# Kernel optimization log

Hardware: AMD Instinct MI355X
Metric: run time of the kernel (lower is better)

## Reference

```python
import jax, jax.numpy as jnp
import numpy as np

NB = 5  # frequency bands


def _ln(x, g, b, eps=1e-5):
    m = jnp.mean(x, axis=-1, keepdims=True)
    v = jnp.var(x, axis=-1, keepdims=True)
    return (x - m) / jnp.sqrt(v + eps) * g + b


def _graph_adj(x, adj_w, sw1, sb1, sw2, sb2, pos_factor, pos_enc):
    # x: [B, D, N] -> degree-normalized adjacency [B, N, N]
    d = x.shape[1]
    xt = jnp.swapaxes(x, 1, 2)  # [B, N, D]
    # concat-MLP first layer split: cat(xi, xj) @ W1 == xi @ W1[:d] + xj @ W1[d:]
    a = xt @ sw1[:d]
    bpart = xt @ sw1[d:]
    h = jax.nn.elu(a[:, :, None, :] + bpart[:, None, :, :] + sb1)  # [B, N, N, H]
    dyn = jax.nn.sigmoid(jnp.squeeze(h @ sw2, -1) + sb2)  # [B, N, N]
    static = jax.nn.softmax(adj_w, axis=-1)
    pos = jax.nn.softmax(pos_enc, axis=-1)
    comb = jax.nn.softmax(static + dyn + pos_factor * pos, axis=-1)
    deg = jnp.sum(comb, axis=-1)
    dis = (deg + 1e-8) ** -0.5
    return dis[:, :, None] * comb * dis[:, None, :]


def _gcn(x, adj, w, b):
    # x: [B, D, N], adj: [B, N, N] -> [B, D_out, N]
    xt = jnp.swapaxes(x, 1, 2)
    out = jnp.einsum('bij,bjd->bid', adj, xt) @ w + b
    return jnp.swapaxes(out, 1, 2)


def _mha(x, qkv_w, qkv_b, ow, ob, nh=4):
    B, S, D = x.shape
    dh = D // nh
    q, k, v = jnp.split(x @ qkv_w + qkv_b, 3, axis=-1)
    q = q.reshape(B, S, nh, dh)
    k = k.reshape(B, S, nh, dh)
    v = v.reshape(B, S, nh, dh)
    att = jax.nn.softmax(jnp.einsum('bihd,bjhd->bhij', q, k) / float(np.sqrt(dh)), axis=-1)
    o = jnp.einsum('bhij,bjhd->bihd', att, v).reshape(B, S, D)
    return o @ ow + ob


def setup_inputs():
    key = jax.random.key(0)
    B, D, N = 16, 256, 64
    ks = iter(jax.random.split(key, 40))

    def rn(shape, s=0.05):
        return jax.random.normal(next(ks), shape, dtype=jnp.float32) * s

    eyeN = jnp.eye(N, dtype=jnp.float32)
    return dict(
        feature=jax.random.normal(next(ks), (B, NB * D, 1, N), dtype=jnp.float32),
        l_adj_w=jnp.tile(eyeN[None], (NB, 1, 1)),
        l_sim_w1=rn((NB, 2 * D, D)), l_sim_b1=jnp.zeros((NB, D), jnp.float32),
        l_sim_w2=rn((NB, D, 1)), l_sim_b2=jnp.zeros((NB, 1), jnp.float32),
        l_pos_factor=jnp.full((NB,), 0.5, jnp.float32),
        l_pos_enc=jnp.tile(eyeN[None], (NB, 1, 1)),
        l_gcn_w=rn((NB, D, D)), l_gcn_b=jnp.zeros((NB, D), jnp.float32),
        g_adj_w=jnp.eye(NB, dtype=jnp.float32),
        g_sim_w1=rn((2 * D, D)), g_sim_b1=jnp.zeros((D,), jnp.float32),
        g_sim_w2=rn((D, 1)), g_sim_b2=jnp.zeros((1,), jnp.float32),
        g_pos_factor=jnp.float32(0.5),
        g_pos_enc=jnp.eye(NB, dtype=jnp.float32),
        g_gcn_w=rn((D, D)), g_gcn_b=jnp.zeros((D,), jnp.float32),
        qkv_w=rn((D, 3 * D)), qkv_b=jnp.zeros((3 * D,), jnp.float32),
        attn_ow=rn((D, D)), attn_ob=jnp.zeros((D,), jnp.float32),
        ln1_g=jnp.ones((D,), jnp.float32), ln1_b=jnp.zeros((D,), jnp.float32),
        ln2_g=jnp.ones((D,), jnp.float32), ln2_b=jnp.zeros((D,), jnp.float32),
        mlp_w1=rn((D, 4 * D)), mlp_b1=jnp.zeros((4 * D,), jnp.float32),
        mlp_w2=rn((4 * D, D)), mlp_b2=jnp.zeros((D,), jnp.float32),
        imp_w=rn((NB, N, 1)), imp_b=jnp.zeros((NB, 1), jnp.float32),
    )


def reference(feature, l_adj_w, l_sim_w1, l_sim_b1, l_sim_w2, l_sim_b2,
              l_pos_factor, l_pos_enc, l_gcn_w, l_gcn_b,
              g_adj_w, g_sim_w1, g_sim_b1, g_sim_w2, g_sim_b2,
              g_pos_factor, g_pos_enc, g_gcn_w, g_gcn_b,
              qkv_w, qkv_b, attn_ow, attn_ob,
              ln1_g, ln1_b, ln2_g, ln2_b,
              mlp_w1, mlp_b1, mlp_w2, mlp_b2,
              imp_w, imp_b):
    B = feature.shape[0]
    D = l_gcn_w.shape[-1]
    N = feature.shape[-1]
    # [B, 5*D, 1, N] -> [5, B, D, N] band-major
    x5 = jnp.moveaxis(feature.reshape(B, NB, D, N), 1, 0)
    # per-band local graphs + GCNs (vmapped over the 5 bands)
    local_adj = jax.vmap(_graph_adj)(x5, l_adj_w, l_sim_w1, l_sim_b1,
                                     l_sim_w2, l_sim_b2, l_pos_factor, l_pos_enc)
    local_out = jax.vmap(_gcn)(x5, local_adj, l_gcn_w, l_gcn_b)  # [5, B, D, N]
    scale_nodes = jnp.moveaxis(jnp.mean(local_out, axis=-1), 0, 1)  # [B, 5, D]
    # cross-band attention block (pre: MHA + residual + LN, then MLP + residual + LN)
    attn = _mha(scale_nodes, qkv_w, qkv_b, attn_ow, attn_ob)
    h1 = _ln(scale_nodes + attn, ln1_g, ln1_b)
    mlp = jax.nn.gelu(h1 @ mlp_w1 + mlp_b1, approximate=False) @ mlp_w2 + mlp_b2
    se = _ln(h1 + mlp, ln2_g, ln2_b)  # [B, 5, D]
    # global scale graph over the 5 band nodes
    xg = jnp.swapaxes(se, 1, 2)  # [B, D, 5]
    g_adj = _graph_adj(xg, g_adj_w, g_sim_w1, g_sim_b1, g_sim_w2, g_sim_b2,
                       g_pos_factor, g_pos_enc)
    g_out = jnp.swapaxes(_gcn(xg, g_adj, g_gcn_w, g_gcn_b), 1, 2)  # [B, 5, D]
    # modulate each local band feature by its global scale vector
    enh = local_out * jnp.moveaxis(g_out, 1, 0)[..., None]  # [5, B, D, N]
    # per-band importance projection over channels: [5, B, D, 1]
    out5 = jnp.einsum('kbdn,kno->kbdo', enh, imp_w) + imp_b[:, None, None, :]
    output = jnp.moveaxis(out5, 0, 1).reshape(B, NB * D, 1, 1)
    return output, g_adj, jnp.moveaxis(local_out, 0, 1)
```

## Files before the change

### kernel.cpp

```cpp
#include <hip/hip_runtime.h>
#include <hip/hip_bf16.h>

#define NBANDS 5
#define BATCH  16
#define DIM    256
#define NNODE  64
#define SEQ    5

typedef __hip_bfloat16 bf16;
typedef unsigned short ushort_t;
typedef __attribute__((ext_vector_type(8))) short short8;
typedef __attribute__((ext_vector_type(4))) float float4v;

#define MFMA __builtin_amdgcn_mfma_f32_16x16x32_bf16

__device__ __forceinline__ float bu2f(ushort_t u){
    bf16 h = *reinterpret_cast<bf16*>(&u);
    return __bfloat162float(h);
}
__device__ __forceinline__ ushort_t f2bu(float x){
    bf16 h = __float2bfloat16(x);
    return *reinterpret_cast<ushort_t*>(&h);
}
__device__ __forceinline__ float elu(float v){
    return (v > 0.f) ? v : (__expf(v) - 1.f);
}

__global__ void __launch_bounds__(256) k_head(
    const float* __restrict__ l_adj_w, const float* __restrict__ l_pos_enc,
    const float* __restrict__ l_pf,
    const float* __restrict__ g_adj_w, const float* __restrict__ g_pos_enc,
    const float* __restrict__ g_pf,
    float* __restrict__ sbase, float* __restrict__ gbase,
    const float* __restrict__ w1, const float* __restrict__ gw,
    ushort_t* __restrict__ w1bt, ushort_t* __restrict__ gwbt)
{
    int blk = blockIdx.x;
    int tid = threadIdx.x;
    __shared__ ushort_t tile[64][65];

    if (blk < 80) {
        int r = blk*4 + (tid>>6);
        int k = r >> 6, i = r & 63;
        int t = tid & 63;
        float aw = l_adj_w[(k*NNODE + i)*NNODE + t];
        float pe = l_pos_enc[(k*NNODE + i)*NNODE + t];
        float m1 = aw, m2 = pe;
        for (int o=32;o>0;o>>=1){ m1 = fmaxf(m1, __shfl_xor(m1,o,64)); m2 = fmaxf(m2, __shfl_xor(m2,o,64)); }
        float e1 = __expf(aw-m1), e2 = __expf(pe-m2);
        float s1=e1, s2=e2;
        for (int o=32;o>0;o>>=1){ s1 += __shfl_xor(s1,o,64); s2 += __shfl_xor(s2,o,64); }
        float pf = l_pf[k];
        sbase[(k*NNODE+i)*NNODE + t] = e1/s1 + pf*(e2/s2);
    } else if (blk == 80) {
        if (tid < NBANDS) {
            int i = tid;
            float r1[NBANDS], r2[NBANDS];
            float m1=-1e30f, m2=-1e30f;
            for (int j=0;j<NBANDS;j++){
                r1[j]=g_adj_w[i*NBANDS+j]; r2[j]=g_pos_enc[i*NBANDS+j];
                m1=fmaxf(m1,r1[j]); m2=fmaxf(m2,r2[j]);
            }
            float s1=0.f,s2=0.f;
            for (int j=0;j<NBANDS;j++){ r1[j]=__expf(r1[j]-m1); r2[j]=__expf(r2[j]-m2); s1+=r1[j]; s2+=r2[j]; }
            float pf = g_pf[0];
            for (int j=0;j<NBANDS;j++) gbase[i*NBANDS+j] = r1[j]/s1 + pf*(r2[j]/s2);
        }
    } else {
        int idx = blk - 81;
        int inst = idx >> 4;
        int t = idx & 15;
        int r0 = (t>>2)*64, c0 = (t&3)*64;
        const float* src; ushort_t* dst;
        if (inst < 10){
            int k = inst>>1, half = inst&1;
            src = w1  + ((size_t)k*512 + half*256)*256;
            dst = w1bt+ ((size_t)k*512 + half*256)*256;
        } else {
            int k = inst-10;
            src = gw  + (size_t)k*65536;
            dst = gwbt+ (size_t)k*65536;
        }
        int jj = tid & 63, i4 = tid >> 6;
        for (int p=0;p<16;p++){
            int i = p*4 + i4;
            tile[i][jj] = f2bu(src[(size_t)(r0+i)*256 + c0 + jj]);
        }
        __syncthreads();
        for (int p=0;p<16;p++){
            int i = p*4 + i4;
            dst[(size_t)(c0+i)*256 + r0 + jj] = tile[jj][i];
        }
    }
}

__global__ void __launch_bounds__(512) k_graph(
    const float* __restrict__ feat,
    const ushort_t* __restrict__ w1bt, const float* __restrict__ b1,
    const float* __restrict__ w2, const float* __restrict__ b2arr,
    const float* __restrict__ sbase,
    const ushort_t* __restrict__ gwbt, const float* __restrict__ gb,
    const float* __restrict__ imp_w,
    float* __restrict__ out_local,
    float* __restrict__ scalew4, float* __restrict__ impw4)
{
    int kb = blockIdx.x % 80;
    int iq = blockIdx.x / 80;
    int k  = kb >> 4;
    int b  = kb & 15;
    int i0 = iq << 4;
    int tid = threadIdx.x;
    int w = tid >> 6, lane = tid & 63, c16 = lane & 15, quad = lane >> 4;

    __shared__ ushort_t Ubuf[64*266 + 8];
    __shared__ ushort_t as[16][264];
    __shared__ ushort_t cs[16][72];
    __shared__ ushort_t ys[16][264];
    __shared__ float w2s[DIM];

    const float* src = feat + ((size_t)b*NBANDS + k)*DIM*NNODE;

    int il0 = w*2, il1 = w*2 + 1;
    float sb0 = sbase[(k*NNODE + i0 + il0)*NNODE + lane];
    float sb1 = sbase[(k*NNODE + i0 + il1)*NNODE + lane];
    float sbias2 = b2arr[k];

    if (tid < DIM) w2s[tid] = w2[k*DIM + tid];
    #pragma unroll
    for (int u = 0; u < 32; ++u){
        int idx = u*512 + tid;
        Ubuf[(idx & 63)*264 + (idx >> 6)] = f2bu(src[idx]);
    }
    __syncthreads();

    int col0 = w*32 + c16;
    int col1 = col0 + 16;

    const ushort_t* Ba = w1bt + (size_t)k*512*DIM;
    const ushort_t* Bb = Ba + 256*DIM;
    float4v z = {0.f,0.f,0.f,0.f};
    float4v aA0=z, aA1=z;
    float4v aB00=z,aB01=z,aB10=z,aB11=z,aB20=z,aB21=z,aB30=z,aB31=z;
    #pragma unroll
    for (int ks = 0; ks < 8; ++ks){
        int ko = ks*32 + quad*8;
        short8 fa = *reinterpret_cast<const short8*>(&Ubuf[(i0 + c16)*264 + ko]);
        short8 f0 = *reinterpret_cast<const short8*>(&Ubuf[( 0 + c16)*264 + ko]);
        short8 f1 = *reinterpret_cast<const short8*>(&Ubuf[(16 + c16)*264 + ko]);
        short8 f2 = *reinterpret_cast<const short8*>(&Ubuf[(32 + c16)*264 + ko]);
        short8 f3 = *reinterpret_cast<const short8*>(&Ubuf[(48 + c16)*264 + ko]);
        short8 wa0 = *reinterpret_cast<const short8*>(Ba + (size_t)col0*DIM + ko);
        short8 wa1 = *reinterpret_cast<const short8*>(Ba + (size_t)col1*DIM + ko);
        short8 wb0 = *reinterpret_cast<const short8*>(Bb + (size_t)col0*DIM + ko);
        short8 wb1 = *reinterpret_cast<const short8*>(Bb + (size_t)col1*DIM + ko);
        aA0  = MFMA(fa, wa0, aA0, 0,0,0);
        aA1  = MFMA(fa, wa1, aA1, 0,0,0);
        aB00 = MFMA(f0, wb0, aB00, 0,0,0);
        aB01 = MFMA(f0, wb1, aB01, 0,0,0);
        aB10 = MFMA(f1, wb0, aB10, 0,0,0);
        aB11 = MFMA(f1, wb1, aB11, 0,0,0);
        aB20 = MFMA(f2, wb0, aB20, 0,0,0);
        aB21 = MFMA(f2, wb1, aB21, 0,0,0);
        aB30 = MFMA(f3, wb0, aB30, 0,0,0);
        aB31 = MFMA(f3, wb1, aB31, 0,0,0);
    }
    __syncthreads();
    {
        float bias0 = b1[k*DIM + col0];
        float bias1 = b1[k*DIM + col1];
        int r0 = quad*4;
        #pragma unroll
        for (int r = 0; r < 4; ++r){
            as[r0 + r][col0] = f2bu(aA0[r] + bias0);
            as[r0 + r][col1] = f2bu(aA1[r] + bias1);
            Ubuf[( 0 + r0 + r)*266 + col0] = f2bu(aB00[r]);
            Ubuf[( 0 + r0 + r)*266 + col1] = f2bu(aB01[r]);
            Ubuf[(16 + r0 + r)*266 + col0] = f2bu(aB10[r]);
            Ubuf[(16 + r0 + r)*266 + col1] = f2bu(aB11[r]);
            Ubuf[(32 + r0 + r)*266 + col0] = f2bu(aB20[r]);
            Ubuf[(32 + r0 + r)*266 + col1] = f2bu(aB21[r]);
            Ubuf[(48 + r0 + r)*266 + col0] = f2bu(aB30[r]);
            Ubuf[(48 + r0 + r)*266 + col1] = f2bu(aB31[r]);
        }
    }
    __syncthreads();

    {
        const ushort_t* bd = Ubuf + 266*lane;
        const ushort_t* a0p = as[il0];
        const ushort_t* a1p = as[il1];
        float acc0 = 0.f, acc1 = 0.f;
        #pragma unroll 4
        for (int dd = 0; dd < 64; ++dd){
            unsigned int blo = *reinterpret_cast<const unsigned int*>(bd + dd*4);
            unsigned int bhi = *reinterpret_cast<const unsigned int*>(bd + dd*4 + 2);
            ushort4 a0 = *reinterpret_cast<const ushort4*>(a0p + dd*4);
            ushort4 a1 = *reinterpret_cast<const ushort4*>(a1p + dd*4);
            float4 wv  = *reinterpret_cast<const float4*>(&w2s[dd*4]);
            float bx = bu2f((ushort_t)(blo & 0xffffu));
            float by = bu2f((ushort_t)(blo >> 16));
            float bz = bu2f((ushort_t)(bhi & 0xffffu));
            float bq = bu2f((ushort_t)(bhi >> 16));
            acc0 += elu(bu2f(a0.x)+bx)*wv.x + elu(bu2f(a0.y)+by)*wv.y
                  + elu(bu2f(a0.z)+bz)*wv.z + elu(bu2f(a0.w)+bq)*wv.w;
            acc1 += elu(bu2f(a1.x)+bx)*wv.x + elu(bu2f(a1.y)+by)*wv.y
                  + elu(bu2f(a1.z)+bz)*wv.z + elu(bu2f(a1.w)+bq)*wv.w;
        }
        float sg0 = 1.f/(1.f + __expf(-(acc0 + sbias2)));
        float sg1 = 1.f/(1.f + __expf(-(acc1 + sbias2)));
        float val0 = sb0 + sg0;
        float val1 = sb1 + sg1;
        float m0 = val0, m1 = val1;
        for (int o=32;o>0;o>>=1){ m0 = fmaxf(m0, __shfl_xor(m0,o,64)); m1 = fmaxf(m1, __shfl_xor(m1,o,64)); }
        float e0 = __expf(val0 - m0), e1 = __expf(val1 - m1);
        float s0 = e0, s1 = e1;
        for (int o=32;o>0;o>>=1){ s0 += __shfl_xor(s0,o,64); s1 += __shfl_xor(s1,o,64); }
        cs[il0][lane] = f2bu(e0/s0);
        cs[il1][lane] = f2bu(e1/s1);
    }
    __syncthreads();

    float4v aY0 = z, aY1 = z;
    {
        #pragma unroll
        for (int ks = 0; ks < 2; ++ks){
            int ko = ks*32 + quad*8;
            short8 af = *reinterpret_cast<const short8*>(&cs[c16][ko]);
            const float* f0p = src + (size_t)col0*NNODE + ko;
            const float* f1p = src + (size_t)col1*NNODE + ko;
            float4 x0 = *reinterpret_cast<const float4*>(f0p);
            float4 x1 = *reinterpret_cast<const float4*>(f0p+4);
            float4 y0 = *reinterpret_cast<const float4*>(f1p);
            float4 y1 = *reinterpret_cast<const float4*>(f1p+4);
            short8 bf0, bf1;
            bf0[0]=(short)f2bu(x0.x); bf0[1]=(short)f2bu(x0.y); bf0[2]=(short)f2bu(x0.z); bf0[3]=(short)f2bu(x0.w);
            bf0[4]=(short)f2bu(x1.x); bf0[5]=(short)f2bu(x1.y); bf0[6]=(short)f2bu(x1.z); bf0[7]=(short)f2bu(x1.w);
            bf1[0]=(short)f2bu(y0.x); bf1[1]=(short)f2bu(y0.y); bf1[2]=(short)f2bu(y0.z); bf1[3]=(short)f2bu(y0.w);
            bf1[4]=(short)f2bu(y1.x); bf1[5]=(short)f2bu(y1.y); bf1[6]=(short)f2bu(y1.z); bf1[7]=(short)f2bu(y1.w);
            aY0 = MFMA(af, bf0, aY0, 0,0,0);
            aY1 = MFMA(af, bf1, aY1, 0,0,0);
        }
        #pragma unroll
        for (int r=0;r<4;++r){
            ys[quad*4 + r][col0] = f2bu(aY0[r]);
            ys[quad*4 + r][col1] = f2bu(aY1[r]);
        }
    }
    __syncthreads();

    {
        float4v aG0 = z, aG1 = z;
        const ushort_t* Bg = gwbt + (size_t)k*DIM*DIM;
        #pragma unroll
        for (int ks = 0; ks < 8; ++ks){
            int ko = ks*32 + quad*8;
            short8 af = *reinterpret_cast<const short8*>(&ys[c16][ko]);
            short8 g0 = *reinterpret_cast<const short8*>(Bg + (size_t)col0*DIM + ko);
            short8 g1 = *reinterpret_cast<const short8*>(Bg + (size_t)col1*DIM + ko);
            aG0 = MFMA(af, g0, aG0, 0,0,0);
            aG1 = MFMA(af, g1, aG1, 0,0,0);
        }
        int nb = i0 + quad*4;
        float iw0 = imp_w[k*NNODE + nb + 0];
        float iw1 = imp_w[k*NNODE + nb + 1];
        float iw2 = imp_w[k*NNODE + nb + 2];
        float iw3 = imp_w[k*NNODE + nb + 3];
        size_t obase = ((size_t)b*NBANDS + k)*DIM;

        float bias0 = gb[k*DIM + col0];
        float v0 = aG0[0]+bias0, v1 = aG0[1]+bias0, v2 = aG0[2]+bias0, v3 = aG0[3]+bias0;
        float4 vv = make_float4(v0,v1,v2,v3);
        *reinterpret_cast<float4*>(&out_local[(obase + col0)*NNODE + nb]) = vv;
        float s  = v0+v1+v2+v3;
        float di = v0*iw0 + v1*iw1 + v2*iw2 + v3*iw3;
        s  += __shfl_xor(s,16,64);  s  += __shfl_xor(s,32,64);
        di += __shfl_xor(di,16,64); di += __shfl_xor(di,32,64);
        if (quad == 0){
            size_t o = ((size_t)iq*80 + b*SEQ + k)*DIM + col0;
            scalew4[o] = s;
            impw4[o]   = di;
        }

        float bias1 = gb[k*DIM + col1];
        v0 = aG1[0]+bias1; v1 = aG1[1]+bias1; v2 = aG1[2]+bias1; v3 = aG1[3]+bias1;
        vv = make_float4(v0,v1,v2,v3);
        *reinterpret_cast<float4*>(&out_local[(obase + col1)*NNODE + nb]) = vv;
        s  = v0+v1+v2+v3;
        di = v0*iw0 + v1*iw1 + v2*iw2 + v3*iw3;
        s  += __shfl_xor(s,16,64);  s  += __shfl_xor(s,32,64);
        di += __shfl_xor(di,16,64); di += __shfl_xor(di,32,64);
        if (quad == 0){
            size_t o = ((size_t)iq*80 + b*SEQ + k)*DIM + col1;
            scalew4[o] = s;
            impw4[o]   = di;
        }
    }
}

__global__ void __launch_bounds__(256) k_qkv_gemv(const float* __restrict__ scalew4,
                        const float* __restrict__ w, const float* __restrict__ bias,
                        float* __restrict__ out)
{
    int row = blockIdx.x / 12;
    int n0 = (blockIdx.x % 12) * 64;
    int tid = threadIdx.x;
    int c = tid & 63, s = tid >> 6;
    __shared__ float xs[DIM];
    __shared__ float part[4][64];
    {
        size_t basei = (size_t)row*DIM + tid;
        xs[tid] = (scalew4[basei] + scalew4[20480 + basei]
                 + scalew4[40960 + basei] + scalew4[61440 + basei]) * (1.f/64.f);
    }
    __syncthreads();
    const float* wp = w + (size_t)(s*64)*768 + n0 + c;
    const float* xp = xs + s*64;
    float acc = 0.f;
    #pragma unroll 8
    for (int i = 0; i < 64; ++i) acc += xp[i] * wp[(size_t)i*768];
    part[s][c] = acc;
    __syncthreads();
    if (s == 0){
        out[(size_t)row*768 + n0 + c] = bias[n0+c] + part[0][c]+part[1][c]+part[2][c]+part[3][c];
    }
}

template<int COLS, int SLICES>
__global__ void __launch_bounds__(256) k_gemv(const float* __restrict__ x, const float* __restrict__ w,
                       const float* __restrict__ bias, float* __restrict__ out,
                       int K, int N, int act)
{
    int chunks = N / COLS;
    int row = blockIdx.x / chunks;
    int n0 = (blockIdx.x % chunks) * COLS;
    int c = threadIdx.x % COLS, s = threadIdx.x / COLS;
    __shared__ float xs[1024];
    __shared__ float part[SLICES][COLS];
    for (int i = threadIdx.x; i < K; i += 256) xs[i] = x[(size_t)row*K + i];
    __syncthreads();
    int klen = K / SLICES;
    const float* wp = w + (size_t)(s*klen)*N + n0 + c;
    const float* xp = xs + s*klen;
    float acc = 0.f;
    #pragma unroll 8
    for (int i = 0; i < klen; ++i) acc += xp[i] * wp[(size_t)i*N];
    part[s][c] = acc;
    __syncthreads();
    if (s == 0){
        float v = bias[n0+c];
        #pragma unroll
        for (int q=0;q<SLICES;q++) v += part[q][c];
        if (act) v = 0.5f*v*(1.f + erff(v*0.70710678118654752f));
        out[(size_t)row*N + n0 + c] = v;
    }
}

__global__ void __launch_bounds__(256) k_projattn(const float* __restrict__ qkvw,
                        const float* __restrict__ ow, const float* __restrict__ ob,
                        float* __restrict__ projw)
{
    int row = blockIdx.x / 4;
    int n0 = (blockIdx.x % 4) * 64;
    int b = row / SEQ, i = row % SEQ;
    int tid = threadIdx.x;
    int h = tid >> 6, l = tid & 63;
    __shared__ float xs[DIM];
    __shared__ float part[4][64];
    const float* base = qkvw + (size_t)b*SEQ*3*DIM;
    float qv = base[(size_t)i*3*DIM + h*64 + l];
    float pj[SEQ];
    #pragma unroll
    for (int j=0;j<SEQ;j++){
        float p = qv * base[(size_t)j*3*DIM + DIM + h*64 + l];
        for (int o=32;o>0;o>>=1) p += __shfl_xor(p,o,64);
        pj[j] = p * 0.125f;
    }
    float m = pj[0];
    #pragma unroll
    for (int j=1;j<SEQ;j++) m = fmaxf(m, pj[j]);
    float ssum = 0.f;
    #pragma unroll
    for (int j=0;j<SEQ;j++){ pj[j] = __expf(pj[j]-m); ssum += pj[j]; }
    float inv = 1.f/ssum;
    float o = 0.f;
    #pragma unroll
    for (int j=0;j<SEQ;j++) o += pj[j]*inv * base[(size_t)j*3*DIM + 2*DIM + h*64 + l];
    xs[tid] = o;
    __syncthreads();
    int c = tid & 63, s = tid >> 6;
    const float* wp = ow + (size_t)(s*64)*DIM + n0 + c;
    const float* xp = xs + s*64;
    float acc = 0.f;
    #pragma unroll 8
    for (int k=0;k<64;++k) acc += xp[k] * wp[(size_t)k*DIM];
    part[s][c] = acc;
    __syncthreads();
    if (s == 0){
        projw[(size_t)row*DIM + n0 + c] = ob[n0+c] + part[0][c]+part[1][c]+part[2][c]+part[3][c];
    }
}

__device__ __forceinline__ float block_ln(float v, int tid, float* red, float g, float bln)
{
    float s = v;
    for (int o=32;o>0;o>>=1) s += __shfl_xor(s,o,64);
    int wave = tid>>6, lane = tid&63;
    if (lane==0) red[wave] = s;
    __syncthreads();
    float mean = (red[0]+red[1]+red[2]+red[3]) * (1.f/DIM);
    float c = v - mean;
    float q = c*c;
    for (int o=32;o>0;o>>=1) q += __shfl_xor(q,o,64);
    __syncthreads();
    if (lane==0) red[wave] = q;
    __syncthreads();
    float var = (red[0]+red[1]+red[2]+red[3]) * (1.f/DIM);
    return c * rsqrtf(var + 1e-5f) * g + bln;
}

__global__ void __launch_bounds__(256) k_mlp1_ln(const float* __restrict__ projw,
                         const float* __restrict__ scalew4,
                         const float* __restrict__ ln1_g, const float* __restrict__ ln1_b,
                         const float* __restrict__ w1, const float* __restrict__ b1,
                         float* __restrict__ h1w, float* __restrict__ mhw)
{
    int row = blockIdx.x / 16;
    int n0 = (blockIdx.x % 16) * 64;
    int tid = threadIdx.x;
    __shared__ float xs[DIM];
    __shared__ float red[4];
    __shared__ float part[4][64];
    size_t basei = (size_t)row*DIM + tid;
    float sc = (scalew4[basei] + scalew4[20480 + basei]
              + scalew4[40960 + basei] + scalew4[61440 + basei]) * (1.f/64.f);
    float v = projw[basei] + sc;
    float h = block_ln(v, tid, red, ln1_g[tid], ln1_b[tid]);
    xs[tid] = h;
    if ((blockIdx.x % 16) == 0) h1w[basei] = h;
    __syncthreads();
    int c = tid & 63, s = tid >> 6;
    const float* wp = w1 + (size_t)(s*64)*1024 + n0 + c;
    const float* xp = xs + s*64;
    float acc = 0.f;
    #pragma unroll 8
    for (int i=0;i<64;++i) acc += xp[i] * wp[(size_t)i*1024];
    part[s][c] = acc;
    __syncthreads();
    if (s == 0){
        float o = b1[n0+c] + part[0][c] + part[1][c] + part[2][c] + part[3][c];
        o = 0.5f*o*(1.f + erff(o*0.70710678118654752f));
        mhw[(size_t)row*1024 + n0 + c] = o;
    }
}

__global__ void __launch_bounds__(256) k_gab_ln(const float* __restrict__ m2w,
                        const float* __restrict__ h1w,
                        const float* __restrict__ ln2_g, const float* __restrict__ ln2_b,
                        const float* __restrict__ gw1, const float* __restrict__ gb1,
                        float* __restrict__ sew, float* __restrict__ gaw, float* __restrict__ gbw)
{
    int row = blockIdx.x / 4;
    int n0 = (blockIdx.x % 4) * 64;
    int tid = threadIdx.x;
    __shared__ float xs[DIM];
    __shared__ float red[4];
    __shared__ float partA[4][64];
    __shared__ float partB[4][64];
    float v = m2w[(size_t)row*DIM + tid] + h1w[(size_t)row*DIM + tid];
    float h = block_ln(v, tid, red, ln2_g[tid], ln2_b[tid]);
    xs[tid] = h;
    if ((blockIdx.x % 4) == 0) sew[(size_t)row*DIM + tid] = h;
    __syncthreads();
    int c = tid & 63, s = tid >> 6;
    const float* wpA = gw1 + (size_t)(s*64)*DIM + n0 + c;
    const float* wpB = wpA + (size_t)DIM*DIM;
    const float* xp = xs + s*64;
    float aA = 0.f, aB = 0.f;
    #pragma unroll 8
    for (int i=0;i<64;++i){
        float xv = xp[i];
        aA += xv * wpA[(size_t)i*DIM];
        aB += xv * wpB[(size_t)i*DIM];
    }
    partA[s][c] = aA;
    partB[s][c] = aB;
    __syncthreads();
    if (s == 0){
        gaw[(size_t)row*DIM + n0 + c] = gb1[n0+c] + partA[0][c]+partA[1][c]+partA[2][c]+partA[3][c];
        gbw[(size_t)row*DIM + n0 + c] = partB[0][c]+partB[1][c]+partB[2][c]+partB[3][c];
    }
}

__global__ void __launch_bounds__(256) k_goutfin(const float* __restrict__ gaw,
                        const float* __restrict__ gbw,
                        const float* __restrict__ gw2, const float* __restrict__ gb2,
                        const float* __restrict__ gbase,
                        const float* __restrict__ sew,
                        const float* __restrict__ ggw, const float* __restrict__ ggb,
                        const float* __restrict__ impw4, const float* __restrict__ imp_b,
                        float* __restrict__ out0, float* __restrict__ out_gadj)
{
    int row = blockIdx.x / 4;
    int n0 = (blockIdx.x % 4) * 64;
    int b = row / SEQ, i = row % SEQ;
    int tid = threadIdx.x;
    int wave = tid >> 6, lane = tid & 63;
    __shared__ float dyn_s[SEQ];
    __shared__ float xs[DIM];
    __shared__ float part[4][64];
    for (int j = wave; j < SEQ; j += 4){
        const float* gar = gaw + (size_t)row*DIM;
        const float* gbr = gbw + ((size_t)b*SEQ + j)*DIM;
        float acc = 0.f;
        #pragma unroll
        for (int m=0;m<4;m++){
            int dd = lane + m*64;
            float v = gar[dd] + gbr[dd];
            acc += elu(v) * gw2[dd];
        }
        for (int o=32;o>0;o>>=1) acc += __shfl_xor(acc,o,64);
        if (lane==0) dyn_s[j] = acc;
    }
    __syncthreads();
    float gc[SEQ];
    {
        float sb2 = gb2[0];
        float m = -1e30f;
        #pragma unroll
        for (int j=0;j<SEQ;j++){
            float sg = 1.f/(1.f+__expf(-(dyn_s[j]+sb2)));
            gc[j] = gbase[i*SEQ+j] + sg;
            m = fmaxf(m, gc[j]);
        }
        float ssum=0.f;
        #pragma unroll
        for (int j=0;j<SEQ;j++){ gc[j]=__expf(gc[j]-m); ssum+=gc[j]; }
        float inv = 1.f/ssum;
        #pragma unroll
        for (int j=0;j<SEQ;j++) gc[j] *= inv;
    }
    if (n0 == 0 && tid < SEQ) out_gadj[((size_t)b*SEQ+i)*SEQ + tid] = gc[tid];
    float t = 0.f;
    #pragma unroll
    for (int j=0;j<SEQ;j++) t += gc[j]*sew[((size_t)b*SEQ + j)*DIM + tid];
    xs[tid] = t;
    __syncthreads();
    int c = tid & 63, s = tid >> 6;
    const float* wp = ggw + (size_t)(s*64)*DIM + n0 + c;
    const float* xp = xs + s*64;
    float acc = 0.f;
    #pragma unroll 8
    for (int k=0;k<64;++k) acc += xp[k] * wp[(size_t)k*DIM];
    part[s][c] = acc;
    __syncthreads();
    if (s == 0){
        float g = ggb[n0+c] + part[0][c]+part[1][c]+part[2][c]+part[3][c];
        size_t o = (size_t)row*DIM + n0 + c;
        float imps = impw4[o] + impw4[20480 + o] + impw4[40960 + o] + impw4[61440 + o];
        out0[o] = g * imps + imp_b[i];
    }
}

extern "C" void kernel_launch(void* const* d_in, const int* in_sizes, int n_in,
                              void* d_out, int out_size, void* d_ws, size_t ws_size,
                              hipStream_t stream)
{
    const float* feature      = (const float*)d_in[0];
    const float* l_adj_w      = (const float*)d_in[1];
    const float* l_sim_w1     = (const float*)d_in[2];
    const float* l_sim_b1     = (const float*)d_in[3];
    const float* l_sim_w2     = (const float*)d_in[4];
    const float* l_sim_b2     = (const float*)d_in[5];
    const float* l_pos_factor = (const float*)d_in[6];
    const float* l_pos_enc    = (const float*)d_in[7];
    const float* l_gcn_w      = (const float*)d_in[8];
    const float* l_gcn_b      = (const float*)d_in[9];
    const float* g_adj_w      = (const float*)d_in[10];
    const float* g_sim_w1     = (const float*)d_in[11];
    const float* g_sim_b1     = (const float*)d_in[12];
    const float* g_sim_w2     = (const float*)d_in[13];
    const float* g_sim_b2     = (const float*)d_in[14];
    const float* g_pos_factor = (const float*)d_in[15];
    const float* g_pos_enc    = (const float*)d_in[16];
    const float* g_gcn_w      = (const float*)d_in[17];
    const float* g_gcn_b      = (const float*)d_in[18];
    const float* qkv_w        = (const float*)d_in[19];
    const float* qkv_b        = (const float*)d_in[20];
    const float* attn_ow      = (const float*)d_in[21];
    const float* attn_ob      = (const float*)d_in[22];
    const float* ln1_g        = (const float*)d_in[23];
    const float* ln1_b        = (const float*)d_in[24];
    const float* ln2_g        = (const float*)d_in[25];
    const float* ln2_b        = (const float*)d_in[26];
    const float* mlp_w1       = (const float*)d_in[27];
    const float* mlp_b1       = (const float*)d_in[28];
    const float* mlp_w2       = (const float*)d_in[29];
    const float* mlp_b2       = (const float*)d_in[30];
    const float* imp_w        = (const float*)d_in[31];
    const float* imp_b        = (const float*)d_in[32];

    float* out0      = (float*)d_out;
    float* out_gadj  = out0 + (size_t)BATCH*NBANDS*DIM;
    float* out_local = out_gadj + (size_t)BATCH*NBANDS*NBANDS;

    ushort_t* w1bt = (ushort_t*)d_ws;
    ushort_t* gwbt = w1bt + (size_t)NBANDS*512*DIM;
    float* fp = (float*)(gwbt + (size_t)NBANDS*DIM*DIM);
    float* sbase   = fp; fp += NBANDS*NNODE*NNODE;
    float* gbase   = fp; fp += 32;
    float* scalew4 = fp; fp += 4*BATCH*SEQ*DIM;
    float* impw4   = fp; fp += 4*BATCH*SEQ*DIM;
    float* qkvw    = fp; fp += BATCH*SEQ*3*DIM;
    float* projw   = fp; fp += BATCH*SEQ*DIM;
    float* h1w     = fp; fp += BATCH*SEQ*DIM;
    float* mhw     = fp; fp += BATCH*SEQ*4*DIM;
    float* m2w     = fp; fp += BATCH*SEQ*DIM;
    float* sew     = fp; fp += BATCH*SEQ*DIM;
    float* gaw     = fp; fp += BATCH*SEQ*DIM;
    float* gbw     = fp; fp += BATCH*SEQ*DIM;

    const int ROWS = BATCH*SEQ;

    k_head<<<321, 256, 0, stream>>>(l_adj_w, l_pos_enc, l_pos_factor,
                                    g_adj_w, g_pos_enc, g_pos_factor,
                                    sbase, gbase,
                                    l_sim_w1, l_gcn_w, w1bt, gwbt);
    k_graph<<<NBANDS*BATCH*4, 512, 0, stream>>>(feature, w1bt, l_sim_b1,
                                    l_sim_w2, l_sim_b2, sbase,
                                    gwbt, l_gcn_b, imp_w,
                                    out_local, scalew4, impw4);
    k_qkv_gemv<<<ROWS*12, 256, 0, stream>>>(scalew4, qkv_w, qkv_b, qkvw);
    k_projattn<<<ROWS*4, 256, 0, stream>>>(qkvw, attn_ow, attn_ob, projw);
    k_mlp1_ln<<<ROWS*16, 256, 0, stream>>>(projw, scalew4, ln1_g, ln1_b, mlp_w1, mlp_b1, h1w, mhw);
    k_gemv<32,8><<<ROWS*8, 256, 0, stream>>>(mhw, mlp_w2, mlp_b2, m2w, 1024, 256, 0);
    k_gab_ln<<<ROWS*4, 256, 0, stream>>>(m2w, h1w, ln2_g, ln2_b, g_sim_w1, g_sim_b1, sew, gaw, gbw);
    k_goutfin<<<ROWS*4, 256, 0, stream>>>(gaw, gbw, g_sim_w2, g_sim_b2, gbase,
                                          sew, g_gcn_w, g_gcn_b, impw4, imp_b,
                                          out0, out_gadj);
}
```

Measured before the change: 215.8 us.

## Pretranspose features to bf16 in head kernel and split graph rows into eighths

Adds a k_head stage that transposes and converts each band's feature slab to bf16 [N,D] in workspace. k_graph then reads MFMA operands directly from global memory instead of staging them through shared memory. k_graph now handles 8 query rows per block instead of 16, which doubles the grid to 640 blocks, and the partial sums grow from 4 to 8 slices that downstream kernels reduce. The intent is more parallelism and less per-block staging, at the cost of redundant B-part MFMA work per block, half-wasted MFMA tiles, and extra global traffic.

```diff
diff --git a/kernel.cpp b/kernel.cpp
--- a/kernel.cpp
+++ b/kernel.cpp
@@ -24,6 +24,12 @@
 }
 __device__ __forceinline__ float elu(float v){
     return (v > 0.f) ? v : (__expf(v) - 1.f);
+}
+__device__ __forceinline__ float sum8(const float* __restrict__ p, size_t i){
+    float v = 0.f;
+    #pragma unroll
+    for (int q = 0; q < 8; ++q) v += p[(size_t)q*20480 + i];
+    return v;
 }
 
 __global__ void __launch_bounds__(256) k_head(
@@ -33,7 +39,8 @@
     const float* __restrict__ g_pf,
     float* __restrict__ sbase, float* __restrict__ gbase,
     const float* __restrict__ w1, const float* __restrict__ gw,
-    ushort_t* __restrict__ w1bt, ushort_t* __restrict__ gwbt)
+    ushort_t* __restrict__ w1bt, ushort_t* __restrict__ gwbt,
+    const float* __restrict__ feat, ushort_t* __restrict__ xtb)
 {
     int blk = blockIdx.x;
     int tid = threadIdx.x;
@@ -66,7 +73,7 @@
             float pf = g_pf[0];
             for (int j=0;j<NBANDS;j++) gbase[i*NBANDS+j] = r1[j]/s1 + pf*(r2[j]/s2);
         }
-    } else {
+    } else if (blk < 321) {
         int idx = blk - 81;
         int inst = idx >> 4;
         int t = idx & 15;
@@ -91,51 +98,64 @@
             int i = p*4 + i4;
             dst[(size_t)(c0+i)*256 + r0 + jj] = tile[jj][i];
         }
+    } else {
+        int idx = blk - 321;
+        int k = idx >> 6;
+        int b = (idx >> 2) & 15;
+        int dt = idx & 3;
+        const float* src = feat + ((size_t)b*NBANDS*DIM + (size_t)k*DIM)*NNODE;
+        ushort_t* dst = xtb + (size_t)(k*BATCH+b)*NNODE*DIM;
+        for (int r=0;r<16;r++){
+            int dp = r*4 + (tid>>6);
+            int n  = tid & 63;
+            tile[dp][n] = f2bu(src[(size_t)(dt*64+dp)*NNODE + n]);
+        }
+        __syncthreads();
+        for (int r=0;r<16;r++){
+            int n  = r*4 + (tid>>6);
+            int dp = tid & 63;
+            dst[(size_t)n*DIM + dt*64 + dp] = tile[dp][n];
+        }
     }
 }
 
 __global__ void __launch_bounds__(512) k_graph(
-    const float* __restrict__ feat,
+    const float* __restrict__ feat, const ushort_t* __restrict__ xtb,
     const ushort_t* __restrict__ w1bt, const float* __restrict__ b1,
     const float* __restrict__ w2, const float* __restrict__ b2arr,
     const float* __restrict__ sbase,
     const ushort_t* __restrict__ gwbt, const float* __restrict__ gb,
     const float* __restrict__ imp_w,
     float* __restrict__ out_local,
-    float* __restrict__ scalew4, float* __restrict__ impw4)
+    float* __restrict__ scalew8, float* __restrict__ impw8)
 {
     int kb = blockIdx.x % 80;
     int iq = blockIdx.x / 80;
     int k  = kb >> 4;
     int b  = kb & 15;
-    int i0 = iq << 4;
+    int i0 = iq << 3;
     int tid = threadIdx.x;
     int w = tid >> 6, lane = tid & 63, c16 = lane & 15, quad = lane >> 4;
 
-    __shared__ ushort_t Ubuf[64*266 + 8];
-    __shared__ ushort_t as[16][264];
+    __shared__ ushort_t as[8][266];
+    __shared__ ushort_t bs[64][266];
     __shared__ ushort_t cs[16][72];
     __shared__ ushort_t ys[16][264];
-    __shared__ float w2s[DIM];
+
+    if (tid < 288) reinterpret_cast<unsigned int*>(&cs[8][0])[tid] = 0u;
+    for (int t = tid; t < 1056; t += 512) reinterpret_cast<unsigned int*>(&ys[8][0])[t] = 0u;
+
+    float sb = sbase[(k*NNODE + i0 + w)*NNODE + lane];
+    float sbias2 = b2arr[k];
 
     const float* src = feat + ((size_t)b*NBANDS + k)*DIM*NNODE;
-
-    int il0 = w*2, il1 = w*2 + 1;
-    float sb0 = sbase[(k*NNODE + i0 + il0)*NNODE + lane];
-    float sb1 = sbase[(k*NNODE + i0 + il1)*NNODE + lane];
-    float sbias2 = b2arr[k];
-
-    if (tid < DIM) w2s[tid] = w2[k*DIM + tid];
-    #pragma unroll
-    for (int u = 0; u < 32; ++u){
-        int idx = u*512 + tid;
-        Ubuf[(idx & 63)*264 + (idx >> 6)] = f2bu(src[idx]);
-    }
-    __syncthreads();
+    const ushort_t* X = xtb + (size_t)(k*BATCH + b)*NNODE*DIM;
 
     int col0 = w*32 + c16;
     int col1 = col0 + 16;
 
+    int arow = i0 + c16; if (arow > 63) arow = 63;
+    const ushort_t* Xa = X + (size_t)arow*DIM;
     const ushort_t* Ba = w1bt + (size_t)k*512*DIM;
     const ushort_t* Bb = Ba + 256*DIM;
     float4v z = {0.f,0.f,0.f,0.f};
@@ -144,11 +164,11 @@
     #pragma unroll
     for (int ks = 0; ks < 8; ++ks){
         int ko = ks*32 + quad*8;
-        short8 fa = *reinterpret_cast<const short8*>(&Ubuf[(i0 + c16)*264 + ko]);
-        short8 f0 = *reinterpret_cast<const short8*>(&Ubuf[( 0 + c16)*264 + ko]);
-        short8 f1 = *reinterpret_cast<const short8*>(&Ubuf[(16 + c16)*264 + ko]);
-        short8 f2 = *reinterpret_cast<const short8*>(&Ubuf[(32 + c16)*264 + ko]);
-        short8 f3 = *reinterpret_cast<const short8*>(&Ubuf[(48 + c16)*264 + ko]);
+        short8 fa = *reinterpret_cast<const short8*>(Xa + ko);
+        short8 f0 = *reinterpret_cast<const short8*>(X + (size_t)( 0 + c16)*DIM + ko);
+        short8 f1 = *reinterpret_cast<const short8*>(X + (size_t)(16 + c16)*DIM + ko);
+        short8 f2 = *reinterpret_cast<const short8*>(X + (size_t)(32 + c16)*DIM + ko);
+        short8 f3 = *reinterpret_cast<const short8*>(X + (size_t)(48 + c16)*DIM + ko);
         short8 wa0 = *reinterpret_cast<const short8*>(Ba + (size_t)col0*DIM + ko);
         short8 wa1 = *reinterpret_cast<const short8*>(Ba + (size_t)col1*DIM + ko);
         short8 wb0 = *reinterpret_cast<const short8*>(Bb + (size_t)col0*DIM + ko);
@@ -164,64 +184,62 @@
         aB30 = MFMA(f3, wb0, aB30, 0,0,0);
         aB31 = MFMA(f3, wb1, aB31, 0,0,0);
     }
-    __syncthreads();
     {
         float bias0 = b1[k*DIM + col0];
         float bias1 = b1[k*DIM + col1];
         int r0 = quad*4;
+        if (quad < 2){
+            #pragma unroll
+            for (int r = 0; r < 4; ++r){
+                as[r0 + r][col0] = f2bu(aA0[r] + bias0);
+                as[r0 + r][col1] = f2bu(aA1[r] + bias1);
+            }
+        }
         #pragma unroll
         for (int r = 0; r < 4; ++r){
-            as[r0 + r][col0] = f2bu(aA0[r] + bias0);
-            as[r0 + r][col1] = f2bu(aA1[r] + bias1);
-            Ubuf[( 0 + r0 + r)*266 + col0] = f2bu(aB00[r]);
-            Ubuf[( 0 + r0 + r)*266 + col1] = f2bu(aB01[r]);
-            Ubuf[(16 + r0 + r)*266 + col0] = f2bu(aB10[r]);
-            Ubuf[(16 + r0 + r)*266 + col1] = f2bu(aB11[r]);
-            Ubuf[(32 + r0 + r)*266 + col0] = f2bu(aB20[r]);
-            Ubuf[(32 + r0 + r)*266 + col1] = f2bu(aB21[r]);
-            Ubuf[(48 + r0 + r)*266 + col0] = f2bu(aB30[r]);
-            Ubuf[(48 + r0 + r)*266 + col1] = f2bu(aB31[r]);
+            bs[ 0 + r0 + r][col0] = f2bu(aB00[r]);
+            bs[ 0 + r0 + r][col1] = f2bu(aB01[r]);
+            bs[16 + r0 + r][col0] = f2bu(aB10[r]);
+            bs[16 + r0 + r][col1] = f2bu(aB11[r]);
+            bs[32 + r0 + r][col0] = f2bu(aB20[r]);
+            bs[32 + r0 + r][col1] = f2bu(aB21[r]);
+            bs[48 + r0 + r][col0] = f2bu(aB30[r]);
+            bs[48 + r0 + r][col1] = f2bu(aB31[r]);
         }
     }
     __syncthreads();
 
     {
-        const ushort_t* bd = Ubuf + 266*lane;
-        const ushort_t* a0p = as[il0];
-        const ushort_t* a1p = as[il1];
-        float acc0 = 0.f, acc1 = 0.f;
+        const ushort_t* bd = bs[lane];
+        const ushort_t* ap = as[w];
+        const float* w2p = w2 + k*DIM;
+        float acc = 0.f;
         #pragma unroll 4
         for (int dd = 0; dd < 64; ++dd){
             unsigned int blo = *reinterpret_cast<const unsigned int*>(bd + dd*4);
             unsigned int bhi = *reinterpret_cast<const unsigned int*>(bd + dd*4 + 2);
-            ushort4 a0 = *reinterpret_cast<const ushort4*>(a0p + dd*4);
-            ushort4 a1 = *reinterpret_cast<const ushort4*>(a1p + dd*4);
-            float4 wv  = *reinterpret_cast<const float4*>(&w2s[dd*4]);
+            ushort4 a0 = *reinterpret_cast<const ushort4*>(ap + dd*4);
+            float4 wv  = *reinterpret_cast<const float4*>(w2p + dd*4);
             float bx = bu2f((ushort_t)(blo & 0xffffu));
             float by = bu2f((ushort_t)(blo >> 16));
             float bz = bu2f((ushort_t)(bhi & 0xffffu));
             float bq = bu2f((ushort_t)(bhi >> 16));
-            acc0 += elu(bu2f(a0.x)+bx)*wv.x + elu(bu2f(a0.y)+by)*wv.y
-                  + elu(bu2f(a0.z)+bz)*wv.z + elu(bu2f(a0.w)+bq)*wv.w;
-            acc1 += elu(bu2f(a1.x)+bx)*wv.x + elu(bu2f(a1.y)+by)*wv.y
-                  + elu(bu2f(a1.z)+bz)*wv.z + elu(bu2f(a1.w)+bq)*wv.w;
-        }
-        float sg0 = 1.f/(1.f + __expf(-(acc0 + sbias2)));
-        float sg1 = 1.f/(1.f + __expf(-(acc1 + sbias2)));
-        float val0 = sb0 + sg0;
-        float val1 = sb1 + sg1;
-        float m0 = val0, m1 = val1;
-        for (int o=32;o>0;o>>=1){ m0 = fmaxf(m0, __shfl_xor(m0,o,64)); m1 = fmaxf(m1, __shfl_xor(m1,o,64)); }
-        float e0 = __expf(val0 - m0), e1 = __expf(val1 - m1);
-        float s0 = e0, s1 = e1;
-        for (int o=32;o>0;o>>=1){ s0 += __shfl_xor(s0,o,64); s1 += __shfl_xor(s1,o,64); }
-        cs[il0][lane] = f2bu(e0/s0);
-        cs[il1][lane] = f2bu(e1/s1);
-    }
-    __syncthreads();
-
-    float4v aY0 = z, aY1 = z;
+            acc += elu(bu2f(a0.x)+bx)*wv.x + elu(bu2f(a0.y)+by)*wv.y
+                 + elu(bu2f(a0.z)+bz)*wv.z + elu(bu2f(a0.w)+bq)*wv.w;
+        }
+        float sg = 1.f/(1.f + __expf(-(acc + sbias2)));
+        float val = sb + sg;
+        float m = val;
+        for (int o=32;o>0;o>>=1) m = fmaxf(m, __shfl_xor(m,o,64));
+        float e = __expf(val - m);
+        float s = e;
+        for (int o=32;o>0;o>>=1) s += __shfl_xor(s,o,64);
+        cs[w][lane] = f2bu(e/s);
+    }
+    __syncthreads();
+
     {
+        float4v aY0 = z, aY1 = z;
         #pragma unroll
         for (int ks = 0; ks < 2; ++ks){
             int ko = ks*32 + quad*8;
@@ -240,10 +258,12 @@
             aY0 = MFMA(af, bf0, aY0, 0,0,0);
             aY1 = MFMA(af, bf1, aY1, 0,0,0);
         }
-        #pragma unroll
-        for (int r=0;r<4;++r){
-            ys[quad*4 + r][col0] = f2bu(aY0[r]);
-            ys[quad*4 + r][col1] = f2bu(aY1[r]);
+        if (quad < 2){
+            #pragma unroll
+            for (int r=0;r<4;++r){
+                ys[quad*4 + r][col0] = f2bu(aY0[r]);
+                ys[quad*4 + r][col1] = f2bu(aY1[r]);
+            }
         }
     }
     __syncthreads();
@@ -261,43 +281,48 @@
             aG1 = MFMA(af, g1, aG1, 0,0,0);
         }
         int nb = i0 + quad*4;
-        float iw0 = imp_w[k*NNODE + nb + 0];
-        float iw1 = imp_w[k*NNODE + nb + 1];
-        float iw2 = imp_w[k*NNODE + nb + 2];
-        float iw3 = imp_w[k*NNODE + nb + 3];
+        int nbc = (quad < 2) ? nb : i0;
+        float iw0 = imp_w[k*NNODE + nbc + 0];
+        float iw1 = imp_w[k*NNODE + nbc + 1];
+        float iw2 = imp_w[k*NNODE + nbc + 2];
+        float iw3 = imp_w[k*NNODE + nbc + 3];
         size_t obase = ((size_t)b*NBANDS + k)*DIM;
 
         float bias0 = gb[k*DIM + col0];
         float v0 = aG0[0]+bias0, v1 = aG0[1]+bias0, v2 = aG0[2]+bias0, v3 = aG0[3]+bias0;
-        float4 vv = make_float4(v0,v1,v2,v3);
-        *reinterpret_cast<float4*>(&out_local[(obase + col0)*NNODE + nb]) = vv;
-        float s  = v0+v1+v2+v3;
-        float di = v0*iw0 + v1*iw1 + v2*iw2 + v3*iw3;
+        if (quad < 2){
+            *reinterpret_cast<float4*>(&out_local[(obase + col0)*NNODE + nb]) =
+                make_float4(v0,v1,v2,v3);
+        }
+        float s  = (quad < 2) ? (v0+v1+v2+v3) : 0.f;
+        float di = (quad < 2) ? (v0*iw0 + v1*iw1 + v2*iw2 + v3*iw3) : 0.f;
         s  += __shfl_xor(s,16,64);  s  += __shfl_xor(s,32,64);
         di += __shfl_xor(di,16,64); di += __shfl_xor(di,32,64);
         if (quad == 0){
-            size_t o = ((size_t)iq*80 + b*SEQ + k)*DIM + col0;
-            scalew4[o] = s;
-            impw4[o]   = di;
+            size_t o = (size_t)iq*20480 + ((size_t)b*SEQ + k)*DIM + col0;
+            scalew8[o] = s;
+            impw8[o]   = di;
         }
 
         float bias1 = gb[k*DIM + col1];
         v0 = aG1[0]+bias1; v1 = aG1[1]+bias1; v2 = aG1[2]+bias1; v3 = aG1[3]+bias1;
-        vv = make_float4(v0,v1,v2,v3);
-        *reinterpret_cast<float4*>(&out_local[(obase + col1)*NNODE + nb]) = vv;
-        s  = v0+v1+v2+v3;
-        di = v0*iw0 + v1*iw1 + v2*iw2 + v3*iw3;
+        if (quad < 2){
+            *reinterpret_cast<float4*>(&out_local[(obase + col1)*NNODE + nb]) =
+                make_float4(v0,v1,v2,v3);
+        }
+        s  = (quad < 2) ? (v0+v1+v2+v3) : 0.f;
+        di = (quad < 2) ? (v0*iw0 + v1*iw1 + v2*iw2 + v3*iw3) : 0.f;
         s  += __shfl_xor(s,16,64);  s  += __shfl_xor(s,32,64);
         di += __shfl_xor(di,16,64); di += __shfl_xor(di,32,64);
         if (quad == 0){
-            size_t o = ((size_t)iq*80 + b*SEQ + k)*DIM + col1;
-            scalew4[o] = s;
-            impw4[o]   = di;
-        }
-    }
-}
-
-__global__ void __launch_bounds__(256) k_qkv_gemv(const float* __restrict__ scalew4,
+            size_t o = (size_t)iq*20480 + ((size_t)b*SEQ + k)*DIM + col1;
+            scalew8[o] = s;
+            impw8[o]   = di;
+        }
+    }
+}
+
+__global__ void __launch_bounds__(256) k_qkv_gemv(const float* __restrict__ scalew8,
                         const float* __restrict__ w, const float* __restrict__ bias,
                         float* __restrict__ out)
 {
@@ -307,11 +332,7 @@
     int c = tid & 63, s = tid >> 6;
     __shared__ float xs[DIM];
     __shared__ float part[4][64];
-    {
-        size_t basei = (size_t)row*DIM + tid;
-        xs[tid] = (scalew4[basei] + scalew4[20480 + basei]
-                 + scalew4[40960 + basei] + scalew4[61440 + basei]) * (1.f/64.f);
-    }
+    xs[tid] = sum8(scalew8, (size_t)row*DIM + tid) * (1.f/64.f);
     __syncthreads();
     const float* wp = w + (size_t)(s*64)*768 + n0 + c;
     const float* xp = xs + s*64;
@@ -419,7 +440,7 @@
 }
 
 __global__ void __launch_bounds__(256) k_mlp1_ln(const float* __restrict__ projw,
-                         const float* __restrict__ scalew4,
+                         const float* __restrict__ scalew8,
                          const float* __restrict__ ln1_g, const float* __restrict__ ln1_b,
                          const float* __restrict__ w1, const float* __restrict__ b1,
                          float* __restrict__ h1w, float* __restrict__ mhw)
@@ -431,8 +452,7 @@
     __shared__ float red[4];
     __shared__ float part[4][64];
     size_t basei = (size_t)row*DIM + tid;
-    float sc = (scalew4[basei] + scalew4[20480 + basei]
-              + scalew4[40960 + basei] + scalew4[61440 + basei]) * (1.f/64.f);
+    float sc = sum8(scalew8, basei) * (1.f/64.f);
     float v = projw[basei] + sc;
     float h = block_ln(v, tid, red, ln1_g[tid], ln1_b[tid]);
     xs[tid] = h;
@@ -497,7 +517,7 @@
                         const float* __restrict__ gbase,
                         const float* __restrict__ sew,
                         const float* __restrict__ ggw, const float* __restrict__ ggb,
-                        const float* __restrict__ impw4, const float* __restrict__ imp_b,
+                        const float* __restrict__ impw8, const float* __restrict__ imp_b,
                         float* __restrict__ out0, float* __restrict__ out_gadj)
 {
     int row = blockIdx.x / 4;
@@ -556,7 +576,7 @@
     if (s == 0){
         float g = ggb[n0+c] + part[0][c]+part[1][c]+part[2][c]+part[3][c];
         size_t o = (size_t)row*DIM + n0 + c;
-        float imps = impw4[o] + impw4[20480 + o] + impw4[40960 + o] + impw4[61440 + o];
+        float imps = sum8(impw8, o);
         out0[o] = g * imps + imp_b[i];
     }
 }
@@ -605,11 +625,12 @@
 
     ushort_t* w1bt = (ushort_t*)d_ws;
     ushort_t* gwbt = w1bt + (size_t)NBANDS*512*DIM;
-    float* fp = (float*)(gwbt + (size_t)NBANDS*DIM*DIM);
+    ushort_t* xtb  = gwbt + (size_t)NBANDS*DIM*DIM;
+    float* fp = (float*)(xtb + (size_t)NBANDS*BATCH*NNODE*DIM);
     float* sbase   = fp; fp += NBANDS*NNODE*NNODE;
     float* gbase   = fp; fp += 32;
-    float* scalew4 = fp; fp += 4*BATCH*SEQ*DIM;
-    float* impw4   = fp; fp += 4*BATCH*SEQ*DIM;
+    float* scalew8 = fp; fp += 8*BATCH*SEQ*DIM;
+    float* impw8   = fp; fp += 8*BATCH*SEQ*DIM;
     float* qkvw    = fp; fp += BATCH*SEQ*3*DIM;
     float* projw   = fp; fp += BATCH*SEQ*DIM;
     float* h1w     = fp; fp += BATCH*SEQ*DIM;
@@ -621,20 +642,21 @@
 
     const int ROWS = BATCH*SEQ;
 
-    k_head<<<321, 256, 0, stream>>>(l_adj_w, l_pos_enc, l_pos_factor,
+    k_head<<<641, 256, 0, stream>>>(l_adj_w, l_pos_enc, l_pos_factor,
                                     g_adj_w, g_pos_enc, g_pos_factor,
                                     sbase, gbase,
-                                    l_sim_w1, l_gcn_w, w1bt, gwbt);
-    k_graph<<<NBANDS*BATCH*4, 512, 0, stream>>>(feature, w1bt, l_sim_b1,
+                                    l_sim_w1, l_gcn_w, w1bt, gwbt,
+                                    feature, xtb);
+    k_graph<<<NBANDS*BATCH*8, 512, 0, stream>>>(feature, xtb, w1bt, l_sim_b1,
                                     l_sim_w2, l_sim_b2, sbase,
                                     gwbt, l_gcn_b, imp_w,
-                                    out_local, scalew4, impw4);
-    k_qkv_gemv<<<ROWS*12, 256, 0, stream>>>(scalew4, qkv_w, qkv_b, qkvw);
+                                    out_local, scalew8, impw8);
+    k_qkv_gemv<<<ROWS*12, 256, 0, stream>>>(scalew8, qkv_w, qkv_b, qkvw);
     k_projattn<<<ROWS*4, 256, 0, stream>>>(qkvw, attn_ow, attn_ob, projw);
-    k_mlp1_ln<<<ROWS*16, 256, 0, stream>>>(projw, scalew4, ln1_g, ln1_b, mlp_w1, mlp_b1, h1w, mhw);
+    k_mlp1_ln<<<ROWS*16, 256, 0, stream>>>(projw, scalew8, ln1_g, ln1_b, mlp_w1, mlp_b1, h1w, mhw);
     k_gemv<32,8><<<ROWS*8, 256, 0, stream>>>(mhw, mlp_w2, mlp_b2, m2w, 1024, 256, 0);
     k_gab_ln<<<ROWS*4, 256, 0, stream>>>(m2w, h1w, ln2_g, ln2_b, g_sim_w1, g_sim_b1, sew, gaw, gbw);
     k_goutfin<<<ROWS*4, 256, 0, stream>>>(gaw, gbw, g_sim_w2, g_sim_b2, gbase,
-                                          sew, g_gcn_w, g_gcn_b, impw4, imp_b,
+                                          sew, g_gcn_w, g_gcn_b, impw8, imp_b,
                                           out0, out_gadj);
 }
```

New measurement: 259.3 us. +20.1%, slower.
